# Optimization experiments

Measured on AMD Instinct MI355X. Metric: run time of the kernel, lower is better.

The kernel has to match this reference:

```python
import jax, jax.numpy as jnp
import numpy as np
from jax import lax

NEG = -1e9  # effective -inf, safe for fp32 and for gradients


def asg_loss(inputs, transitions, targets):
    """ASG criterion (wav2letter / gtn_applications semantics).

    inputs:      [B, T, N] emissions (log scores)
    transitions: [N+1, N]; transitions[0, i] = start score of class i,
                 transitions[i+1, j] = score of transition j -> i
    targets:     [B, L] int class ids (already replabel-packed + garbage-interleaved)
    Returns mean over batch of (logZ - forced_align_score) / L.
    """
    B, T, N = inputs.shape
    L = targets.shape[1]
    init = transitions[0]      # [N]
    trans = transitions[1:]    # [N, N], trans[i, j]: j -> i

    # ---- denominator: free recursion over all label sequences ----
    alpha0 = inputs[:, 0, :] + init  # [B, N]
    emis_t = jnp.swapaxes(inputs, 0, 1)  # [T, B, N]

    def den_step(alpha, e_t):
        # alpha[b, j] -> new alpha[b, i] = e_t[b, i] + LSE_j(alpha[b, j] + trans[i, j])
        a = jax.nn.logsumexp(alpha[:, None, :] + trans[None, :, :], axis=-1) + e_t
        return a, None

    alphaT, _ = lax.scan(den_step, alpha0, emis_t[1:])
    logZ = jax.nn.logsumexp(alphaT, axis=-1)  # [B]

    # ---- numerator: forced-alignment graph (self-loop or advance) ----
    # emissions gathered at target labels: [B, T, L]
    emis_y = jnp.take_along_axis(inputs, jnp.broadcast_to(targets[:, None, :], (B, T, L)), axis=2)
    stay_w = trans[targets, targets]                      # [B, L]   y_s -> y_s
    adv_w = trans[targets[:, 1:], targets[:, :-1]]        # [B, L-1] y_{s-1} -> y_s

    beta0 = jnp.full((B, L), NEG, dtype=inputs.dtype)
    beta0 = beta0.at[:, 0].set(init[targets[:, 0]] + emis_y[:, 0, 0])
    emis_y_t = jnp.swapaxes(emis_y, 0, 1)  # [T, B, L]

    def num_step(beta, e_t):
        stay = beta + stay_w
        adv = jnp.concatenate(
            [jnp.full((B, 1), NEG, dtype=beta.dtype), beta[:, :-1] + adv_w], axis=1)
        b = jnp.logaddexp(stay, adv) + e_t
        return b, None

    betaT, _ = lax.scan(num_step, beta0, emis_y_t[1:])
    target_score = betaT[:, -1]  # must end having consumed all L labels

    # reduction = 'mean': scale each sample by 1/len(target), then batch mean
    return jnp.mean((logZ - target_score) / L)


def setup_inputs() -> dict:
    key = jax.random.key(0)
    k1, k2, k3 = jax.random.split(key, 3)
    B, T, N, L = 128, 4000, 64, 101
    inputs = jax.random.normal(k1, (B, T, N), dtype=jnp.float32)
    transitions = jax.random.normal(k2, (N + 1, N), dtype=jnp.float32) * 0.1
    targets = jax.random.randint(k3, (B, L), 0, N, dtype=jnp.int64)
    return {"inputs": inputs, "transitions": transitions, "targets": targets}


def reference(inputs, transitions, targets):
    return asg_loss(inputs, transitions, targets)
```

## Files before the change

### kernel.cpp

```cpp
#include <hip/hip_runtime.h>


#define TT 4000
#define NN 64
#define LL 101
#define NSEG 64
#define SEGN 62
#define SLOTS 93

static constexpr float L2E  = 1.44269504088896340736f;
static constexpr float LN2F = 0.69314718055994530942f;
static constexpr float NEG2 = -1.0e30f;

#define WS_X    0
#define WS_NF   8192
#define WS_HB   22528
#define WS_LOSS 36864

#if defined(__has_builtin)
#if __has_builtin(__builtin_amdgcn_mfma_f32_16x16x16bf16_1k)
#define BF16MM 1
#endif
#if __has_builtin(__builtin_amdgcn_exp2f)
#define FEXP2(x) __builtin_amdgcn_exp2f(x)
#endif
#if __has_builtin(__builtin_amdgcn_logf)
#define FLOG2(x) __builtin_amdgcn_logf(x)
#endif
#endif
#ifndef FEXP2
#define FEXP2(x) exp2f(x)
#endif
#ifndef FLOG2
#define FLOG2(x) log2f(x)
#endif

typedef float f32x4 __attribute__((ext_vector_type(4)));
typedef short s16x4 __attribute__((ext_vector_type(4)));
typedef _Float16 h4 __attribute__((ext_vector_type(4)));

__device__ __forceinline__ unsigned cvt2(float a, float b) {
#ifdef BF16MM
  const unsigned ua = __builtin_bit_cast(unsigned, a);
  const unsigned ub = __builtin_bit_cast(unsigned, b);
  const unsigned ra = (ua + 0x7FFFu + ((ua >> 16) & 1u)) >> 16;
  const unsigned rb = (ub + 0x7FFFu + ((ub >> 16) & 1u)) >> 16;
  return ra | (rb << 16);
#else
  return __builtin_bit_cast(unsigned,
      __builtin_amdgcn_cvt_pkrtz(fminf(a, 3.0e4f), fminf(b, 3.0e4f)));
#endif
}

__device__ __forceinline__ f32x4 MM(uint2 a, uint2 b, f32x4 c) {
#ifdef BF16MM
  return __builtin_amdgcn_mfma_f32_16x16x16bf16_1k(
      __builtin_bit_cast(s16x4, a), __builtin_bit_cast(s16x4, b), c, 0, 0, 0);
#else
  return __builtin_amdgcn_mfma_f32_16x16x16f16(
      __builtin_bit_cast(h4, a), __builtin_bit_cast(h4, b), c, 0, 0, 0);
#endif
}

template<int CTRL>
__device__ __forceinline__ float dppf(float x) {
  return __builtin_bit_cast(float, __builtin_amdgcn_update_dpp(
      0, __builtin_bit_cast(int, x), CTRL, 0xf, 0xf, true));
}

__global__ __launch_bounds__(128) void asg_den(
    const float* __restrict__ E, const float* __restrict__ TR,
    float* __restrict__ ws)
{
  const int bid  = blockIdx.x;
  const int w    = threadIdx.x >> 6;
  const int lane = threadIdx.x & 63;
  const int b    = bid >> 1;
  const int p    = bid & 1;
  const int g4   = p * 2 + w;
  const float* em = E + (size_t)b * TT * NN;

  const int c = lane & 15, g = lane >> 4;
  const int j = g4 * 16 + c;

  uint2 Af[4][4];
#pragma unroll
  for (int rt = 0; rt < 4; ++rt)
#pragma unroll
    for (int kt = 0; kt < 4; ++kt) {
      const float* tr = TR + (size_t)(16 * rt + c + 1) * NN + 16 * kt + 4 * g;
      Af[rt][kt].x = cvt2(FEXP2(tr[0] * L2E), FEXP2(tr[1] * L2E));
      Af[rt][kt].y = cvt2(FEXP2(tr[2] * L2E), FEXP2(tr[3] * L2E));
    }

  f32x4 P[4];
#pragma unroll
  for (int rt = 0; rt < 4; ++rt)
#pragma unroll
    for (int e = 0; e < 4; ++e) {
      const int row = 16 * rt + 4 * g + e;
      P[rt][e] = (j == 0) ? FEXP2((em[row] + TR[row]) * L2E) : 1.0f;
    }

  float Csum = 0.f, snap = 0.f;
  const float* ebase = em + (size_t)(SEGN * j + 1) * NN + 4 * g;

#define COLSUM(dst) { float t_ =                                               \
    (P[0].x + P[0].y + P[0].z + P[0].w) + (P[1].x + P[1].y + P[1].z + P[1].w)  \
  + (P[2].x + P[2].y + P[2].z + P[2].w) + (P[3].x + P[3].y + P[3].z + P[3].w); \
  t_ += __shfl_xor(t_, 16); t_ += __shfl_xor(t_, 32);                          \
  (dst) = fmaxf(t_, 1e-30f); }

#define RENORM() { float cs_; COLSUM(cs_);                                     \
  const int mb_ = ((__builtin_bit_cast(int, cs_) >> 23) & 255) - 127;          \
  const float sc_ = __builtin_bit_cast(float, (127 - mb_) << 23);              \
  P[0] *= sc_; P[1] *= sc_; P[2] *= sc_; P[3] *= sc_;                          \
  Csum += (float)mb_; }

#define ELOAD(D, s_) { const int se_ = (s_) < (SLOTS - 1) ? (s_) : (SLOTS - 1);\
  const f32x4* p_ = (const f32x4*)(ebase + (size_t)se_ * NN);                  \
  D[0] = p_[0]; D[1] = p_[4]; D[2] = p_[8]; D[3] = p_[12]; }

#define STEP(M)                                                                \
  {                                                                            \
    uint2 Bf[4];                                                               \
    _Pragma("unroll") for (int kt = 0; kt < 4; ++kt) {                         \
      Bf[kt].x = cvt2(P[kt].x, P[kt].y);                                       \
      Bf[kt].y = cvt2(P[kt].z, P[kt].w);                                       \
    }                                                                          \
    _Pragma("unroll") for (int rt = 0; rt < 4; ++rt) {                         \
      f32x4 acc = {0.f, 0.f, 0.f, 0.f};                                        \
      acc = MM(Af[rt][0], Bf[0], acc);                                         \
      acc = MM(Af[rt][1], Bf[1], acc);                                         \
      acc = MM(Af[rt][2], Bf[2], acc);                                         \
      acc = MM(Af[rt][3], Bf[3], acc);                                         \
      _Pragma("unroll") for (int e = 0; e < 4; ++e)                            \
        P[rt][e] = fminf(fmaxf(                                                \
            acc[e] * FEXP2(fmaf(M[rt][e], L2E, -6.7f)), 1e-20f), 1e25f);       \
    }                                                                          \
  }

#define SUB(Ebuf, ss, kr)                                                      \
  { f32x4 T_[4] = {Ebuf[0], Ebuf[1], Ebuf[2], Ebuf[3]};                        \
    ELOAD(Ebuf, (ss) + 6);                                                     \
    STEP(T_);                                                                  \
    if ((ss) == 30) { float cs2_; COLSUM(cs2_);                                \
                      snap = Csum + FLOG2(cs2_) + 6.7f * 31.f; }               \
    if ((kr) == 5) RENORM(); }

  f32x4 E0[4], E1[4], E2[4], E3[4], E4[4], E5[4];
  ELOAD(E0, 0); ELOAD(E1, 1); ELOAD(E2, 2);
  ELOAD(E3, 3); ELOAD(E4, 4); ELOAD(E5, 5);

  for (int it = 0; it < 15; ++it) {
    const int s = 6 * it;
    SUB(E0, s, 0);     SUB(E1, s + 1, 1); SUB(E2, s + 2, 2);
    SUB(E3, s + 3, 3); SUB(E4, s + 4, 4); SUB(E5, s + 5, 5);
  }
  { f32x4 T_[4] = {E0[0], E0[1], E0[2], E0[3]}; STEP(T_); }
  { f32x4 T_[4] = {E1[0], E1[1], E1[2], E1[3]}; STEP(T_); }
  { f32x4 T_[4] = {E2[0], E2[1], E2[2], E2[3]}; STEP(T_); }

  float csf; COLSUM(csf);
  const float fin = Csum + FLOG2(csf) + 6.7f * (float)SLOTS;
  const float X = fin - ((j == 0) ? 0.f : snap);
  if (lane < 16) ws[WS_X + b * NSEG + g4 * 16 + lane] = X;

#undef SUB
#undef STEP
#undef ELOAD
#undef RENORM
#undef COLSUM
}

template<int DIR>
__device__ __forceinline__ void num_chain(const float* __restrict__ em,
                                          const float* __restrict__ TR,
                                          const int* __restrict__ Y,
                                          float* __restrict__ ws,
                                          const int b, const int l)
{
  const bool v0 = (2 * l     <= 100);
  const bool v1 = (2 * l + 1 <= 100);
  const int k0 = v0 ? 2 * l     : 100;
  const int k1 = v1 ? 2 * l + 1 : 100;
  const int y0 = Y[b * LL + k0];
  const int y1 = Y[b * LL + k1];
  const float SW0 = v0 ? FEXP2(TR[(y0 + 1) * NN + y0] * L2E) : 0.f;
  const float SW1 = v1 ? FEXP2(TR[(y1 + 1) * NN + y1] * L2E) : 0.f;
  float WLOC, WRECV, B0, B1, C;
  bool recvok;
  if (DIR == 0) {
    WLOC = v1 ? FEXP2(TR[(y1 + 1) * NN + y0] * L2E) : 0.f;
    const int ym0 = Y[b * LL + (k0 > 0 ? k0 - 1 : 0)];
    recvok = v0 && (l > 0);
    WRECV = recvok ? FEXP2(TR[(y0 + 1) * NN + ym0] * L2E) : 0.f;
    B0 = (l == 0) ? 1.f : 0.f;
    B1 = 0.f;
    C  = (l == 0) ? (TR[y0] + em[y0]) * L2E : 0.f;
  } else {
    WLOC = v1 ? FEXP2(TR[(y1 + 1) * NN + y0] * L2E) : 0.f;
    const int kp = (2 * l + 2 <= 100) ? 2 * l + 2 : 100;
    const int yp1 = Y[b * LL + kp];
    recvok = (2 * l + 2 <= 100);
    WRECV = recvok ? FEXP2(TR[(yp1 + 1) * NN + y1] * L2E) : 0.f;
    B0 = (l == 50) ? 1.f : 0.f;
    B1 = 0.f;
    C  = (l == 50) ? em[(size_t)(TT - 1) * NN + y0] * L2E : 0.f;
  }

#define TROW(t) ((size_t)((DIR == 0) ? (t) : (TT - 1 - (t))) * NN)
#define RADDR(t) em[TROW(((t) < 1999 ? (t) : 1999)) + l]

  float ring[48];
  float PE0[16], PE1[16];
  float ADJ = 0.f;

#define RESCALE()                                                              \
  {                                                                            \
    const float v_ = B0 + B1;                                                  \
    const int bits_ = __builtin_bit_cast(int, v_);                             \
    const int m_ = (v_ > 0.f) ? ((bits_ >> 23) & 255) - 127 : 0;               \
    const float sc_ = __builtin_bit_cast(float, (127 - m_) << 23);             \
    B0 *= sc_; B1 *= sc_; C += (float)m_;                                      \
    const float Cn_ = dppf<(DIR == 0) ? 0x138 : 0x130>(C);                     \
    const float dC_ = fminf(fmaxf(Cn_ - C, -120.f), 120.f);                    \
    ADJ = recvok ? FEXP2(dC_) * WRECV : 0.f;                                   \
  }

#define NSTEP2(E0v, E1v)                                                       \
  {                                                                            \
    if (DIR == 0) {                                                            \
      const float NB = dppf<0x138>(B1);                                        \
      const float t0 = fmaf(NB, ADJ, B0 * SW0);                                \
      const float t1 = fmaf(B0, WLOC, B1 * SW1);                               \
      B0 = t0 * (E0v); B1 = t1 * (E1v);                                        \
    } else {                                                                   \
      const float NB = dppf<0x130>(B0);                                        \
      const float t1 = fmaf(NB, ADJ, B1 * SW1);                                \
      const float t0 = fmaf(B1, WLOC, B0 * SW0);                               \
      B0 = t0 * (E0v); B1 = t1 * (E1v);                                        \
    }                                                                          \
  }

#pragma unroll
  for (int k = 0; k < 48; ++k) ring[(1 + k) % 48] = RADDR(1 + k);
#pragma unroll
  for (int t = 1; t <= 8; ++t) {
    const float r_ = ring[t % 48];
    PE0[t & 15] = FEXP2(__shfl(r_, y0) * L2E);
    PE1[t & 15] = FEXP2(__shfl(r_, y1) * L2E);
  }

#define QSTEP(k)                                                               \
  { if (((k) & 7) == 0) RESCALE();                                             \
    NSTEP2(PE0[(1 + (k)) & 15], PE1[(1 + (k)) & 15]);                          \
    { const float r_ = ring[(1 + (k) + 8) % 48];                               \
      PE0[(1 + (k) + 8) & 15] = FEXP2(__shfl(r_, y0) * L2E);                   \
      PE1[(1 + (k) + 8) & 15] = FEXP2(__shfl(r_, y1) * L2E); }                 \
    ring[(1 + (k)) % 48] = RADDR(tc + (k) + 48); }

#define Q4(k0)  QSTEP(k0) QSTEP((k0) + 1) QSTEP((k0) + 2) QSTEP((k0) + 3)
#define Q16(k0) Q4(k0) Q4((k0) + 4) Q4((k0) + 8) Q4((k0) + 12)

  for (int i = 0; i < 41; ++i) {
    const int tc = 1 + 48 * i;
    Q16(0) Q16(16) Q16(32)
  }
  {
    const int tc = 1969;
    Q16(0)
    Q4(16) Q4(20) Q4(24)
    QSTEP(28) QSTEP(29) QSTEP(30)
  }

#undef Q16
#undef Q4
#undef QSTEP
#undef NSTEP2
#undef RESCALE
#undef RADDR
#undef TROW

  const float o0 = (B0 > 1e-37f) ? C + FLOG2(B0) : NEG2;
  const float o1 = (B1 > 1e-37f) ? C + FLOG2(B1) : NEG2;
  const int base = (DIR ? WS_HB : WS_NF) + b * 112;
  if (v0) ws[base + 2 * l]     = o0;
  if (v1) ws[base + 2 * l + 1] = o1;
}

__global__ __launch_bounds__(64) void asg_num(
    const float* __restrict__ E, const float* __restrict__ TR,
    const int* __restrict__ Y, float* __restrict__ ws)
{
  const int bid = blockIdx.x;
  const int b   = bid >> 1;
  const int dir = bid & 1;
  const float* em = E + (size_t)b * TT * NN;
  if (dir == 0) num_chain<0>(em, TR, Y, ws, b, (int)threadIdx.x);
  else          num_chain<1>(em, TR, Y, ws, b, (int)threadIdx.x);
}

__global__ __launch_bounds__(128) void asg_combine(
    const float* __restrict__ TR, const int* __restrict__ Y,
    const float* __restrict__ ws, float* __restrict__ lossv)
{
  const int b = blockIdx.x;
  const int tid = threadIdx.x;
  __shared__ float sN[LL], sH[LL], red[128];
  __shared__ float sLogZ;

  if (tid == 0) {
    float z = 0.f;
    for (int s = 0; s < NSEG; ++s) z += ws[WS_X + b * NSEG + s];
    sLogZ = z;
  }
  if (tid < LL) { sN[tid] = ws[WS_NF + b * 112 + tid]; sH[tid] = ws[WS_HB + b * 112 + tid]; }
  __syncthreads();

  float val2 = -3.0e38f;
  if (tid < LL) {
    const int l = tid;
    const int y = Y[b * LL + l];
    const float s1 = sN[l] + TR[(y + 1) * NN + y] * L2E;
    float s2 = NEG2;
    if (l > 0) {
      const int ymm = Y[b * LL + l - 1];
      s2 = sN[l - 1] + TR[(y + 1) * NN + ymm] * L2E;
    }
    const float m = fmaxf(s1, s2);
    val2 = m + log2f(exp2f(s1 - m) + exp2f(s2 - m)) + sH[l];
  }
  red[tid] = val2;
  __syncthreads();
  if (tid == 0) {
    float m = red[0];
    for (int k = 1; k < LL; ++k) m = fmaxf(m, red[k]);
    float s = 0.f;
    for (int k = 0; k < LL; ++k) s += exp2f(red[k] - m);
    const float tgt2 = m + log2f(s);
    lossv[b] = (sLogZ - tgt2) * LN2F / (float)LL;
  }
}

__global__ __launch_bounds__(64) void asg_reduce(const float* __restrict__ lossv,
                                                 float* __restrict__ out)
{
  const int tid = threadIdx.x;
  float v = lossv[tid] + lossv[tid + 64];
  for (int off = 32; off; off >>= 1) v += __shfl_xor(v, off);
  if (tid == 0) out[0] = v * (1.0f / 128.0f);
}

extern "C" void kernel_launch(void* const* d_in, const int* in_sizes, int n_in,
                              void* d_out, int out_size, void* d_ws, size_t ws_size,
                              hipStream_t stream) {
  const float* E  = (const float*)d_in[0];
  const float* TR = (const float*)d_in[1];
  const int*   Y  = (const int*)d_in[2];
  float* out = (float*)d_out;
  float* ws  = (float*)d_ws;
  float* lossv = ws + WS_LOSS;

  asg_den<<<dim3(256), dim3(128), 0, stream>>>(E, TR, ws);
  asg_num<<<dim3(256), dim3(64), 0, stream>>>(E, TR, Y, ws);
  asg_combine<<<dim3(128), dim3(128), 0, stream>>>(TR, Y, ws, lossv);
  asg_reduce<<<dim3(1), dim3(64), 0, stream>>>(lossv, out);
}
```

Before: 153.0 us.

## Merge denominator and numerator kernels into one launch, direct-gather numerator loads

Combines the denominator MFMA kernel and the numerator chain kernel into a single 384-block launch. The numerator blocks now run both directions as two wavefronts in one block, so the two phases overlap across the GPU instead of running back to back. The numerator no longer loads full emission rows into a ring and shuffles out the target columns. Each lane now gathers its own two target emissions directly, using triple-buffered batches of 16 timesteps held in named registers. This removes the per-step shuffles and one kernel launch, at the cost of more scattered global loads and higher register pressure under launch_bounds(128,1).

```diff
diff --git a/kernel.cpp b/kernel.cpp
--- a/kernel.cpp
+++ b/kernel.cpp
@@ -66,111 +66,6 @@
 __device__ __forceinline__ float dppf(float x) {
   return __builtin_bit_cast(float, __builtin_amdgcn_update_dpp(
       0, __builtin_bit_cast(int, x), CTRL, 0xf, 0xf, true));
-}
-
-__global__ __launch_bounds__(128) void asg_den(
-    const float* __restrict__ E, const float* __restrict__ TR,
-    float* __restrict__ ws)
-{
-  const int bid  = blockIdx.x;
-  const int w    = threadIdx.x >> 6;
-  const int lane = threadIdx.x & 63;
-  const int b    = bid >> 1;
-  const int p    = bid & 1;
-  const int g4   = p * 2 + w;
-  const float* em = E + (size_t)b * TT * NN;
-
-  const int c = lane & 15, g = lane >> 4;
-  const int j = g4 * 16 + c;
-
-  uint2 Af[4][4];
-#pragma unroll
-  for (int rt = 0; rt < 4; ++rt)
-#pragma unroll
-    for (int kt = 0; kt < 4; ++kt) {
-      const float* tr = TR + (size_t)(16 * rt + c + 1) * NN + 16 * kt + 4 * g;
-      Af[rt][kt].x = cvt2(FEXP2(tr[0] * L2E), FEXP2(tr[1] * L2E));
-      Af[rt][kt].y = cvt2(FEXP2(tr[2] * L2E), FEXP2(tr[3] * L2E));
-    }
-
-  f32x4 P[4];
-#pragma unroll
-  for (int rt = 0; rt < 4; ++rt)
-#pragma unroll
-    for (int e = 0; e < 4; ++e) {
-      const int row = 16 * rt + 4 * g + e;
-      P[rt][e] = (j == 0) ? FEXP2((em[row] + TR[row]) * L2E) : 1.0f;
-    }
-
-  float Csum = 0.f, snap = 0.f;
-  const float* ebase = em + (size_t)(SEGN * j + 1) * NN + 4 * g;
-
-#define COLSUM(dst) { float t_ =                                               \
-    (P[0].x + P[0].y + P[0].z + P[0].w) + (P[1].x + P[1].y + P[1].z + P[1].w)  \
-  + (P[2].x + P[2].y + P[2].z + P[2].w) + (P[3].x + P[3].y + P[3].z + P[3].w); \
-  t_ += __shfl_xor(t_, 16); t_ += __shfl_xor(t_, 32);                          \
-  (dst) = fmaxf(t_, 1e-30f); }
-
-#define RENORM() { float cs_; COLSUM(cs_);                                     \
-  const int mb_ = ((__builtin_bit_cast(int, cs_) >> 23) & 255) - 127;          \
-  const float sc_ = __builtin_bit_cast(float, (127 - mb_) << 23);              \
-  P[0] *= sc_; P[1] *= sc_; P[2] *= sc_; P[3] *= sc_;                          \
-  Csum += (float)mb_; }
-
-#define ELOAD(D, s_) { const int se_ = (s_) < (SLOTS - 1) ? (s_) : (SLOTS - 1);\
-  const f32x4* p_ = (const f32x4*)(ebase + (size_t)se_ * NN);                  \
-  D[0] = p_[0]; D[1] = p_[4]; D[2] = p_[8]; D[3] = p_[12]; }
-
-#define STEP(M)                                                                \
-  {                                                                            \
-    uint2 Bf[4];                                                               \
-    _Pragma("unroll") for (int kt = 0; kt < 4; ++kt) {                         \
-      Bf[kt].x = cvt2(P[kt].x, P[kt].y);                                       \
-      Bf[kt].y = cvt2(P[kt].z, P[kt].w);                                       \
-    }                                                                          \
-    _Pragma("unroll") for (int rt = 0; rt < 4; ++rt) {                         \
-      f32x4 acc = {0.f, 0.f, 0.f, 0.f};                                        \
-      acc = MM(Af[rt][0], Bf[0], acc);                                         \
-      acc = MM(Af[rt][1], Bf[1], acc);                                         \
-      acc = MM(Af[rt][2], Bf[2], acc);                                         \
-      acc = MM(Af[rt][3], Bf[3], acc);                                         \
-      _Pragma("unroll") for (int e = 0; e < 4; ++e)                            \
-        P[rt][e] = fminf(fmaxf(                                                \
-            acc[e] * FEXP2(fmaf(M[rt][e], L2E, -6.7f)), 1e-20f), 1e25f);       \
-    }                                                                          \
-  }
-
-#define SUB(Ebuf, ss, kr)                                                      \
-  { f32x4 T_[4] = {Ebuf[0], Ebuf[1], Ebuf[2], Ebuf[3]};                        \
-    ELOAD(Ebuf, (ss) + 6);                                                     \
-    STEP(T_);                                                                  \
-    if ((ss) == 30) { float cs2_; COLSUM(cs2_);                                \
-                      snap = Csum + FLOG2(cs2_) + 6.7f * 31.f; }               \
-    if ((kr) == 5) RENORM(); }
-
-  f32x4 E0[4], E1[4], E2[4], E3[4], E4[4], E5[4];
-  ELOAD(E0, 0); ELOAD(E1, 1); ELOAD(E2, 2);
-  ELOAD(E3, 3); ELOAD(E4, 4); ELOAD(E5, 5);
-
-  for (int it = 0; it < 15; ++it) {
-    const int s = 6 * it;
-    SUB(E0, s, 0);     SUB(E1, s + 1, 1); SUB(E2, s + 2, 2);
-    SUB(E3, s + 3, 3); SUB(E4, s + 4, 4); SUB(E5, s + 5, 5);
-  }
-  { f32x4 T_[4] = {E0[0], E0[1], E0[2], E0[3]}; STEP(T_); }
-  { f32x4 T_[4] = {E1[0], E1[1], E1[2], E1[3]}; STEP(T_); }
-  { f32x4 T_[4] = {E2[0], E2[1], E2[2], E2[3]}; STEP(T_); }
-
-  float csf; COLSUM(csf);
-  const float fin = Csum + FLOG2(csf) + 6.7f * (float)SLOTS;
-  const float X = fin - ((j == 0) ? 0.f : snap);
-  if (lane < 16) ws[WS_X + b * NSEG + g4 * 16 + lane] = X;
-
-#undef SUB
-#undef STEP
-#undef ELOAD
-#undef RENORM
-#undef COLSUM
 }
 
 template<int DIR>
@@ -209,11 +104,9 @@
     C  = (l == 50) ? em[(size_t)(TT - 1) * NN + y0] * L2E : 0.f;
   }
 
-#define TROW(t) ((size_t)((DIR == 0) ? (t) : (TT - 1 - (t))) * NN)
-#define RADDR(t) em[TROW(((t) < 1999 ? (t) : 1999)) + l]
-
-  float ring[48];
-  float PE0[16], PE1[16];
+  constexpr int ST = (DIR == 0) ? NN : -NN;
+#define TROW0(t) ((long)((DIR == 0) ? (t) : (TT - 1 - (t))) * NN)
+
   float ADJ = 0.f;
 
 #define RESCALE()                                                              \
@@ -243,44 +136,64 @@
     }                                                                          \
   }
 
-#pragma unroll
-  for (int k = 0; k < 48; ++k) ring[(1 + k) % 48] = RADDR(1 + k);
-#pragma unroll
-  for (int t = 1; t <= 8; ++t) {
-    const float r_ = ring[t % 48];
-    PE0[t & 15] = FEXP2(__shfl(r_, y0) * L2E);
-    PE1[t & 15] = FEXP2(__shfl(r_, y1) * L2E);
-  }
-
-#define QSTEP(k)                                                               \
-  { if (((k) & 7) == 0) RESCALE();                                             \
-    NSTEP2(PE0[(1 + (k)) & 15], PE1[(1 + (k)) & 15]);                          \
-    { const float r_ = ring[(1 + (k) + 8) % 48];                               \
-      PE0[(1 + (k) + 8) & 15] = FEXP2(__shfl(r_, y0) * L2E);                   \
-      PE1[(1 + (k) + 8) & 15] = FEXP2(__shfl(r_, y1) * L2E); }                 \
-    ring[(1 + (k)) % 48] = RADDR(tc + (k) + 48); }
-
-#define Q4(k0)  QSTEP(k0) QSTEP((k0) + 1) QSTEP((k0) + 2) QSTEP((k0) + 3)
-#define Q16(k0) Q4(k0) Q4((k0) + 4) Q4((k0) + 8) Q4((k0) + 12)
+#define NB_DECL(Bk)                                                            \
+  float Bk##0a, Bk##0b, Bk##1a, Bk##1b, Bk##2a, Bk##2b, Bk##3a, Bk##3b,        \
+        Bk##4a, Bk##4b, Bk##5a, Bk##5b, Bk##6a, Bk##6b, Bk##7a, Bk##7b,        \
+        Bk##8a, Bk##8b, Bk##9a, Bk##9b, Bk##10a, Bk##10b, Bk##11a, Bk##11b,    \
+        Bk##12a, Bk##12b, Bk##13a, Bk##13b, Bk##14a, Bk##14b, Bk##15a, Bk##15b;
+
+  NB_DECL(KA) NB_DECL(KB) NB_DECL(KC)
+
+#define NLD(Bk, k)                                                             \
+  Bk##k##a = p0_[(k) * ST];                                                    \
+  Bk##k##b = p1_[(k) * ST];
+
+#define NISSUE(Bk, ts)                                                         \
+  { const float* p0_ = em + TROW0(ts) + y0;                                    \
+    const float* p1_ = em + TROW0(ts) + y1;                                    \
+    NLD(Bk,0)  NLD(Bk,1)  NLD(Bk,2)  NLD(Bk,3)                                 \
+    NLD(Bk,4)  NLD(Bk,5)  NLD(Bk,6)  NLD(Bk,7)                                 \
+    NLD(Bk,8)  NLD(Bk,9)  NLD(Bk,10) NLD(Bk,11)                                \
+    NLD(Bk,12) NLD(Bk,13) NLD(Bk,14) NLD(Bk,15) }
+
+#define NRUN1(Bk, k)                                                           \
+  { const float E0_ = FEXP2(Bk##k##a * L2E);                                   \
+    const float E1_ = FEXP2(Bk##k##b * L2E);                                   \
+    NSTEP2(E0_, E1_); }
+
+#define NRUN8A(Bk) RESCALE();                                                  \
+  NRUN1(Bk,0) NRUN1(Bk,1) NRUN1(Bk,2) NRUN1(Bk,3)                              \
+  NRUN1(Bk,4) NRUN1(Bk,5) NRUN1(Bk,6) NRUN1(Bk,7)
+#define NRUN8B(Bk) RESCALE();                                                  \
+  NRUN1(Bk,8)  NRUN1(Bk,9)  NRUN1(Bk,10) NRUN1(Bk,11)                          \
+  NRUN1(Bk,12) NRUN1(Bk,13) NRUN1(Bk,14) NRUN1(Bk,15)
+#define NRUN16(Bk) NRUN8A(Bk) NRUN8B(Bk)
+
+  NISSUE(KA, 1)
+  NISSUE(KB, 17)
 
   for (int i = 0; i < 41; ++i) {
     const int tc = 1 + 48 * i;
-    Q16(0) Q16(16) Q16(32)
-  }
-  {
-    const int tc = 1969;
-    Q16(0)
-    Q4(16) Q4(20) Q4(24)
-    QSTEP(28) QSTEP(29) QSTEP(30)
-  }
-
-#undef Q16
-#undef Q4
-#undef QSTEP
+    NISSUE(KC, tc + 32)  NRUN16(KA)
+    NISSUE(KA, tc + 48)  NRUN16(KB)
+    NISSUE(KB, tc + 64)  NRUN16(KC)
+  }
+  NRUN16(KA)
+  NRUN8A(KB)
+  RESCALE();
+  NRUN1(KB,8) NRUN1(KB,9) NRUN1(KB,10) NRUN1(KB,11)
+  NRUN1(KB,12) NRUN1(KB,13) NRUN1(KB,14)
+
+#undef NRUN16
+#undef NRUN8B
+#undef NRUN8A
+#undef NRUN1
+#undef NISSUE
+#undef NLD
+#undef NB_DECL
 #undef NSTEP2
 #undef RESCALE
-#undef RADDR
-#undef TROW
+#undef TROW0
 
   const float o0 = (B0 > 1e-37f) ? C + FLOG2(B0) : NEG2;
   const float o1 = (B1 > 1e-37f) ? C + FLOG2(B1) : NEG2;
@@ -289,16 +202,118 @@
   if (v1) ws[base + 2 * l + 1] = o1;
 }
 
-__global__ __launch_bounds__(64) void asg_num(
+__global__ __launch_bounds__(128, 1) void asg_main(
     const float* __restrict__ E, const float* __restrict__ TR,
     const int* __restrict__ Y, float* __restrict__ ws)
 {
-  const int bid = blockIdx.x;
-  const int b   = bid >> 1;
-  const int dir = bid & 1;
-  const float* em = E + (size_t)b * TT * NN;
-  if (dir == 0) num_chain<0>(em, TR, Y, ws, b, (int)threadIdx.x);
-  else          num_chain<1>(em, TR, Y, ws, b, (int)threadIdx.x);
+  const int bid  = blockIdx.x;
+  const int w    = threadIdx.x >> 6;
+  const int lane = threadIdx.x & 63;
+
+  if (bid < 256) {
+    const int b    = bid >> 1;
+    const int p    = bid & 1;
+    const int g4   = p * 2 + w;
+    const float* em = E + (size_t)b * TT * NN;
+
+    const int c = lane & 15, g = lane >> 4;
+    const int j = g4 * 16 + c;
+
+    uint2 Af[4][4];
+#pragma unroll
+    for (int rt = 0; rt < 4; ++rt)
+#pragma unroll
+      for (int kt = 0; kt < 4; ++kt) {
+        const float* tr = TR + (size_t)(16 * rt + c + 1) * NN + 16 * kt + 4 * g;
+        Af[rt][kt].x = cvt2(FEXP2(tr[0] * L2E), FEXP2(tr[1] * L2E));
+        Af[rt][kt].y = cvt2(FEXP2(tr[2] * L2E), FEXP2(tr[3] * L2E));
+      }
+
+    f32x4 P[4];
+#pragma unroll
+    for (int rt = 0; rt < 4; ++rt)
+#pragma unroll
+      for (int e = 0; e < 4; ++e) {
+        const int row = 16 * rt + 4 * g + e;
+        P[rt][e] = (j == 0) ? FEXP2((em[row] + TR[row]) * L2E) : 1.0f;
+      }
+
+    float Csum = 0.f, snap = 0.f;
+    const float* ebase = em + (size_t)(SEGN * j + 1) * NN + 4 * g;
+
+#define COLSUM(dst) { float t_ =                                               \
+    (P[0].x + P[0].y + P[0].z + P[0].w) + (P[1].x + P[1].y + P[1].z + P[1].w)  \
+  + (P[2].x + P[2].y + P[2].z + P[2].w) + (P[3].x + P[3].y + P[3].z + P[3].w); \
+  t_ += __shfl_xor(t_, 16); t_ += __shfl_xor(t_, 32);                          \
+  (dst) = fmaxf(t_, 1e-30f); }
+
+#define RENORM() { float cs_; COLSUM(cs_);                                     \
+  const int mb_ = ((__builtin_bit_cast(int, cs_) >> 23) & 255) - 127;          \
+  const float sc_ = __builtin_bit_cast(float, (127 - mb_) << 23);              \
+  P[0] *= sc_; P[1] *= sc_; P[2] *= sc_; P[3] *= sc_;                          \
+  Csum += (float)mb_; }
+
+#define ELOAD(D, s_) { const int se_ = (s_) < (SLOTS - 1) ? (s_) : (SLOTS - 1);\
+  const f32x4* p_ = (const f32x4*)(ebase + (size_t)se_ * NN);                  \
+  D[0] = p_[0]; D[1] = p_[4]; D[2] = p_[8]; D[3] = p_[12]; }
+
+#define STEP(M)                                                                \
+  {                                                                            \
+    uint2 Bf[4];                                                               \
+    _Pragma("unroll") for (int kt = 0; kt < 4; ++kt) {                         \
+      Bf[kt].x = cvt2(P[kt].x, P[kt].y);                                       \
+      Bf[kt].y = cvt2(P[kt].z, P[kt].w);                                       \
+    }                                                                          \
+    _Pragma("unroll") for (int rt = 0; rt < 4; ++rt) {                         \
+      f32x4 acc = {0.f, 0.f, 0.f, 0.f};                                        \
+      acc = MM(Af[rt][0], Bf[0], acc);                                         \
+      acc = MM(Af[rt][1], Bf[1], acc);                                         \
+      acc = MM(Af[rt][2], Bf[2], acc);                                         \
+      acc = MM(Af[rt][3], Bf[3], acc);                                         \
+      _Pragma("unroll") for (int e = 0; e < 4; ++e)                            \
+        P[rt][e] = fminf(fmaxf(                                                \
+            acc[e] * FEXP2(fmaf(M[rt][e], L2E, -6.7f)), 1e-20f), 1e25f);       \
+    }                                                                          \
+  }
+
+#define SUB(Ebuf, ss, kr)                                                      \
+  { f32x4 T_[4] = {Ebuf[0], Ebuf[1], Ebuf[2], Ebuf[3]};                        \
+    ELOAD(Ebuf, (ss) + 6);                                                     \
+    STEP(T_);                                                                  \
+    if ((ss) == 30) { float cs2_; COLSUM(cs2_);                                \
+                      snap = Csum + FLOG2(cs2_) + 6.7f * 31.f; }               \
+    if ((kr) == 5) RENORM(); }
+
+    f32x4 E0[4], E1[4], E2[4], E3[4], E4[4], E5[4];
+    ELOAD(E0, 0); ELOAD(E1, 1); ELOAD(E2, 2);
+    ELOAD(E3, 3); ELOAD(E4, 4); ELOAD(E5, 5);
+
+    for (int it = 0; it < 15; ++it) {
+      const int s = 6 * it;
+      SUB(E0, s, 0);     SUB(E1, s + 1, 1); SUB(E2, s + 2, 2);
+      SUB(E3, s + 3, 3); SUB(E4, s + 4, 4); SUB(E5, s + 5, 5);
+    }
+    { f32x4 T_[4] = {E0[0], E0[1], E0[2], E0[3]}; STEP(T_); }
+    { f32x4 T_[4] = {E1[0], E1[1], E1[2], E1[3]}; STEP(T_); }
+    { f32x4 T_[4] = {E2[0], E2[1], E2[2], E2[3]}; STEP(T_); }
+
+    float csf; COLSUM(csf);
+    const float fin = Csum + FLOG2(csf) + 6.7f * (float)SLOTS;
+    const float X = fin - ((j == 0) ? 0.f : snap);
+    if (lane < 16) ws[WS_X + b * NSEG + g4 * 16 + lane] = X;
+
+#undef SUB
+#undef STEP
+#undef ELOAD
+#undef RENORM
+#undef COLSUM
+
+  } else {
+    const int b = bid - 256;
+    const float* em = E + (size_t)b * TT * NN;
+    if (w == 0) num_chain<0>(em, TR, Y, ws, b, lane);
+    else        num_chain<1>(em, TR, Y, ws, b, lane);
+  }
 }
 
 __global__ __launch_bounds__(128) void asg_combine(
@@ -362,8 +377,7 @@
   float* ws  = (float*)d_ws;
   float* lossv = ws + WS_LOSS;
 
-  asg_den<<<dim3(256), dim3(128), 0, stream>>>(E, TR, ws);
-  asg_num<<<dim3(256), dim3(64), 0, stream>>>(E, TR, Y, ws);
+  asg_main<<<dim3(384), dim3(128), 0, stream>>>(E, TR, Y, ws);
   asg_combine<<<dim3(128), dim3(128), 0, stream>>>(TR, Y, ws, lossv);
   asg_reduce<<<dim3(1), dim3(64), 0, stream>>>(lossv, out);
 }
```

Measured after the change: 127.9 us. 16.4% less time.

## Fuse denominator and numerator kernels and interleave forward/backward numerator chains

Applied to the files above, without the earlier changes.

Merges the denominator and numerator kernels into one launch of 384 blocks, so the numerator blocks run alongside the denominator blocks instead of after them. Each numerator wave now runs both the forward and backward chains interleaved, which gives two independent dependency chains to hide latency. It gathers emissions directly at the label columns with double-buffered 16-step register loads, replacing the ring buffer plus shuffles. It also swaps round-to-nearest bf16 conversion for truncation and drops the upper clamp in the denominator step, trading some precision and overflow safety for fewer instructions.

```diff
diff --git a/kernel.cpp b/kernel.cpp
--- a/kernel.cpp
+++ b/kernel.cpp
@@ -52,6 +52,17 @@
 #endif
 }
 
+__device__ __forceinline__ unsigned cvt2t(float a, float b) {
+#ifdef BF16MM
+  const unsigned ua = __builtin_bit_cast(unsigned, a);
+  const unsigned ub = __builtin_bit_cast(unsigned, b);
+  return (ua >> 16) | (ub & 0xFFFF0000u);
+#else
+  return __builtin_bit_cast(unsigned,
+      __builtin_amdgcn_cvt_pkrtz(fminf(a, 3.0e4f), fminf(b, 3.0e4f)));
+#endif
+}
+
 __device__ __forceinline__ f32x4 MM(uint2 a, uint2 b, f32x4 c) {
 #ifdef BF16MM
   return __builtin_amdgcn_mfma_f32_16x16x16bf16_1k(
@@ -68,42 +79,44 @@
       0, __builtin_bit_cast(int, x), CTRL, 0xf, 0xf, true));
 }
 
-__global__ __launch_bounds__(128) void asg_den(
+__global__ __launch_bounds__(128, 1) void asg_main(
     const float* __restrict__ E, const float* __restrict__ TR,
-    float* __restrict__ ws)
+    const int* __restrict__ Y, float* __restrict__ ws)
 {
   const int bid  = blockIdx.x;
   const int w    = threadIdx.x >> 6;
   const int lane = threadIdx.x & 63;
-  const int b    = bid >> 1;
-  const int p    = bid & 1;
-  const int g4   = p * 2 + w;
-  const float* em = E + (size_t)b * TT * NN;
-
-  const int c = lane & 15, g = lane >> 4;
-  const int j = g4 * 16 + c;
-
-  uint2 Af[4][4];
+
+  if (bid < 256) {
+    const int b    = bid >> 1;
+    const int p    = bid & 1;
+    const int g4   = p * 2 + w;
+    const float* em = E + (size_t)b * TT * NN;
+
+    const int c = lane & 15, g = lane >> 4;
+    const int j = g4 * 16 + c;
+
+    uint2 Af[4][4];
 #pragma unroll
-  for (int rt = 0; rt < 4; ++rt)
+    for (int rt = 0; rt < 4; ++rt)
 #pragma unroll
-    for (int kt = 0; kt < 4; ++kt) {
-      const float* tr = TR + (size_t)(16 * rt + c + 1) * NN + 16 * kt + 4 * g;
-      Af[rt][kt].x = cvt2(FEXP2(tr[0] * L2E), FEXP2(tr[1] * L2E));
-      Af[rt][kt].y = cvt2(FEXP2(tr[2] * L2E), FEXP2(tr[3] * L2E));
-    }
-
-  f32x4 P[4];
+      for (int kt = 0; kt < 4; ++kt) {
+        const float* tr = TR + (size_t)(16 * rt + c + 1) * NN + 16 * kt + 4 * g;
+        Af[rt][kt].x = cvt2(FEXP2(tr[0] * L2E), FEXP2(tr[1] * L2E));
+        Af[rt][kt].y = cvt2(FEXP2(tr[2] * L2E), FEXP2(tr[3] * L2E));
+      }
+
+    f32x4 P[4];
 #pragma unroll
-  for (int rt = 0; rt < 4; ++rt)
+    for (int rt = 0; rt < 4; ++rt)
 #pragma unroll
-    for (int e = 0; e < 4; ++e) {
-      const int row = 16 * rt + 4 * g + e;
-      P[rt][e] = (j == 0) ? FEXP2((em[row] + TR[row]) * L2E) : 1.0f;
-    }
-
-  float Csum = 0.f, snap = 0.f;
-  const float* ebase = em + (size_t)(SEGN * j + 1) * NN + 4 * g;
+      for (int e = 0; e < 4; ++e) {
+        const int row = 16 * rt + 4 * g + e;
+        P[rt][e] = (j == 0) ? FEXP2((em[row] + TR[row]) * L2E) : 1.0f;
+      }
+
+    float Csum = 0.f, snap = 0.f;
+    const float* ebase = em + (size_t)(SEGN * j + 1) * NN + 4 * g;
 
 #define COLSUM(dst) { float t_ =                                               \
     (P[0].x + P[0].y + P[0].z + P[0].w) + (P[1].x + P[1].y + P[1].z + P[1].w)  \
@@ -125,8 +138,8 @@
   {                                                                            \
     uint2 Bf[4];                                                               \
     _Pragma("unroll") for (int kt = 0; kt < 4; ++kt) {                         \
-      Bf[kt].x = cvt2(P[kt].x, P[kt].y);                                       \
-      Bf[kt].y = cvt2(P[kt].z, P[kt].w);                                       \
+      Bf[kt].x = cvt2t(P[kt].x, P[kt].y);                                      \
+      Bf[kt].y = cvt2t(P[kt].z, P[kt].w);                                      \
     }                                                                          \
     _Pragma("unroll") for (int rt = 0; rt < 4; ++rt) {                         \
       f32x4 acc = {0.f, 0.f, 0.f, 0.f};                                        \
@@ -135,8 +148,7 @@
       acc = MM(Af[rt][2], Bf[2], acc);                                         \
       acc = MM(Af[rt][3], Bf[3], acc);                                         \
       _Pragma("unroll") for (int e = 0; e < 4; ++e)                            \
-        P[rt][e] = fminf(fmaxf(                                                \
-            acc[e] * FEXP2(fmaf(M[rt][e], L2E, -6.7f)), 1e-20f), 1e25f);       \
+        P[rt][e] = fmaxf(acc[e] * FEXP2(fmaf(M[rt][e], L2E, -6.7f)), 1e-20f);  \
     }                                                                          \
   }
 
@@ -148,157 +160,155 @@
                       snap = Csum + FLOG2(cs2_) + 6.7f * 31.f; }               \
     if ((kr) == 5) RENORM(); }
 
-  f32x4 E0[4], E1[4], E2[4], E3[4], E4[4], E5[4];
-  ELOAD(E0, 0); ELOAD(E1, 1); ELOAD(E2, 2);
-  ELOAD(E3, 3); ELOAD(E4, 4); ELOAD(E5, 5);
-
-  for (int it = 0; it < 15; ++it) {
-    const int s = 6 * it;
-    SUB(E0, s, 0);     SUB(E1, s + 1, 1); SUB(E2, s + 2, 2);
-    SUB(E3, s + 3, 3); SUB(E4, s + 4, 4); SUB(E5, s + 5, 5);
-  }
-  { f32x4 T_[4] = {E0[0], E0[1], E0[2], E0[3]}; STEP(T_); }
-  { f32x4 T_[4] = {E1[0], E1[1], E1[2], E1[3]}; STEP(T_); }
-  { f32x4 T_[4] = {E2[0], E2[1], E2[2], E2[3]}; STEP(T_); }
-
-  float csf; COLSUM(csf);
-  const float fin = Csum + FLOG2(csf) + 6.7f * (float)SLOTS;
-  const float X = fin - ((j == 0) ? 0.f : snap);
-  if (lane < 16) ws[WS_X + b * NSEG + g4 * 16 + lane] = X;
+    f32x4 E0[4], E1[4], E2[4], E3[4], E4[4], E5[4];
+    ELOAD(E0, 0); ELOAD(E1, 1); ELOAD(E2, 2);
+    ELOAD(E3, 3); ELOAD(E4, 4); ELOAD(E5, 5);
+
+    for (int it = 0; it < 15; ++it) {
+      const int s = 6 * it;
+      SUB(E0, s, 0);     SUB(E1, s + 1, 1); SUB(E2, s + 2, 2);
+      SUB(E3, s + 3, 3); SUB(E4, s + 4, 4); SUB(E5, s + 5, 5);
+    }
+    { f32x4 T_[4] = {E0[0], E0[1], E0[2], E0[3]}; STEP(T_); }
+    { f32x4 T_[4] = {E1[0], E1[1], E1[2], E1[3]}; STEP(T_); }
+    { f32x4 T_[4] = {E2[0], E2[1], E2[2], E2[3]}; STEP(T_); }
+
+    float csf; COLSUM(csf);
+    const float fin = Csum + FLOG2(csf) + 6.7f * (float)SLOTS;
+    const float X = fin - ((j == 0) ? 0.f : snap);
+    if (lane < 16) ws[WS_X + b * NSEG + g4 * 16 + lane] = X;
 
 #undef SUB
 #undef STEP
 #undef ELOAD
 #undef RENORM
 #undef COLSUM
-}
-
-template<int DIR>
-__device__ __forceinline__ void num_chain(const float* __restrict__ em,
-                                          const float* __restrict__ TR,
-                                          const int* __restrict__ Y,
-                                          float* __restrict__ ws,
-                                          const int b, const int l)
-{
-  const bool v0 = (2 * l     <= 100);
-  const bool v1 = (2 * l + 1 <= 100);
-  const int k0 = v0 ? 2 * l     : 100;
-  const int k1 = v1 ? 2 * l + 1 : 100;
-  const int y0 = Y[b * LL + k0];
-  const int y1 = Y[b * LL + k1];
-  const float SW0 = v0 ? FEXP2(TR[(y0 + 1) * NN + y0] * L2E) : 0.f;
-  const float SW1 = v1 ? FEXP2(TR[(y1 + 1) * NN + y1] * L2E) : 0.f;
-  float WLOC, WRECV, B0, B1, C;
-  bool recvok;
-  if (DIR == 0) {
-    WLOC = v1 ? FEXP2(TR[(y1 + 1) * NN + y0] * L2E) : 0.f;
+
+  } else {
+    if (w != 0) return;
+    const int b = bid - 256;
+    const int l = lane;
+    const float* em = E + (size_t)b * TT * NN;
+
+    const bool v0 = (2 * l     <= 100);
+    const bool v1 = (2 * l + 1 <= 100);
+    const int k0 = v0 ? 2 * l     : 100;
+    const int k1 = v1 ? 2 * l + 1 : 100;
+    const int y0 = Y[b * LL + k0];
+    const int y1 = Y[b * LL + k1];
+    const float SW0 = v0 ? FEXP2(TR[(y0 + 1) * NN + y0] * L2E) : 0.f;
+    const float SW1 = v1 ? FEXP2(TR[(y1 + 1) * NN + y1] * L2E) : 0.f;
+    const float WLOC = v1 ? FEXP2(TR[(y1 + 1) * NN + y0] * L2E) : 0.f;
+
     const int ym0 = Y[b * LL + (k0 > 0 ? k0 - 1 : 0)];
-    recvok = v0 && (l > 0);
-    WRECV = recvok ? FEXP2(TR[(y0 + 1) * NN + ym0] * L2E) : 0.f;
-    B0 = (l == 0) ? 1.f : 0.f;
-    B1 = 0.f;
-    C  = (l == 0) ? (TR[y0] + em[y0]) * L2E : 0.f;
-  } else {
-    WLOC = v1 ? FEXP2(TR[(y1 + 1) * NN + y0] * L2E) : 0.f;
+    const bool frecv = v0 && (l > 0);
+    const float FWRECV = frecv ? FEXP2(TR[(y0 + 1) * NN + ym0] * L2E) : 0.f;
+    float FB0 = (l == 0) ? 1.f : 0.f;
+    float FB1 = 0.f;
+    float FC  = (l == 0) ? (TR[y0] + em[y0]) * L2E : 0.f;
+    float FADJ = 0.f;
+
     const int kp = (2 * l + 2 <= 100) ? 2 * l + 2 : 100;
     const int yp1 = Y[b * LL + kp];
-    recvok = (2 * l + 2 <= 100);
-    WRECV = recvok ? FEXP2(TR[(yp1 + 1) * NN + y1] * L2E) : 0.f;
-    B0 = (l == 50) ? 1.f : 0.f;
-    B1 = 0.f;
-    C  = (l == 50) ? em[(size_t)(TT - 1) * NN + y0] * L2E : 0.f;
-  }
-
-#define TROW(t) ((size_t)((DIR == 0) ? (t) : (TT - 1 - (t))) * NN)
-#define RADDR(t) em[TROW(((t) < 1999 ? (t) : 1999)) + l]
-
-  float ring[48];
-  float PE0[16], PE1[16];
-  float ADJ = 0.f;
-
-#define RESCALE()                                                              \
-  {                                                                            \
-    const float v_ = B0 + B1;                                                  \
+    const bool grecv = (2 * l + 2 <= 100);
+    const float GWRECV = grecv ? FEXP2(TR[(yp1 + 1) * NN + y1] * L2E) : 0.f;
+    float GB0 = (l == 50) ? 1.f : 0.f;
+    float GB1 = 0.f;
+    float GC  = (l == 50) ? em[(size_t)(TT - 1) * NN + y0] * L2E : 0.f;
+    float GADJ = 0.f;
+
+#define FOR16(M, P) M(P,0) M(P,1) M(P,2) M(P,3) M(P,4) M(P,5) M(P,6) M(P,7)    \
+                    M(P,8) M(P,9) M(P,10) M(P,11) M(P,12) M(P,13) M(P,14) M(P,15)
+#define DECL1(P, k) float P##k##a, P##k##b;
+    FOR16(DECL1, FA) FOR16(DECL1, FB) FOR16(DECL1, GA) FOR16(DECL1, GB)
+
+#define LDF1(P, k) P##k##a = q0_[(k) * NN]; P##k##b = q1_[(k) * NN];
+#define ISSF(P, ts) { const float* q0_ = em + (size_t)(ts) * NN + y0;          \
+                      const float* q1_ = em + (size_t)(ts) * NN + y1;          \
+                      FOR16(LDF1, P) }
+#define LDG1(P, k) P##k##a = q0_[-(k) * NN]; P##k##b = q1_[-(k) * NN];
+#define ISSG(P, ts) { const float* q0_ = em + (size_t)(TT - 1 - (ts)) * NN + y0;\
+                      const float* q1_ = em + (size_t)(TT - 1 - (ts)) * NN + y1;\
+                      FOR16(LDG1, P) }
+
+#define FRESC()                                                                \
+  { const float v_ = FB0 + FB1;                                                \
     const int bits_ = __builtin_bit_cast(int, v_);                             \
     const int m_ = (v_ > 0.f) ? ((bits_ >> 23) & 255) - 127 : 0;               \
     const float sc_ = __builtin_bit_cast(float, (127 - m_) << 23);             \
-    B0 *= sc_; B1 *= sc_; C += (float)m_;                                      \
-    const float Cn_ = dppf<(DIR == 0) ? 0x138 : 0x130>(C);                     \
-    const float dC_ = fminf(fmaxf(Cn_ - C, -120.f), 120.f);                    \
-    ADJ = recvok ? FEXP2(dC_) * WRECV : 0.f;                                   \
-  }
-
-#define NSTEP2(E0v, E1v)                                                       \
-  {                                                                            \
-    if (DIR == 0) {                                                            \
-      const float NB = dppf<0x138>(B1);                                        \
-      const float t0 = fmaf(NB, ADJ, B0 * SW0);                                \
-      const float t1 = fmaf(B0, WLOC, B1 * SW1);                               \
-      B0 = t0 * (E0v); B1 = t1 * (E1v);                                        \
-    } else {                                                                   \
-      const float NB = dppf<0x130>(B0);                                        \
-      const float t1 = fmaf(NB, ADJ, B1 * SW1);                                \
-      const float t0 = fmaf(B1, WLOC, B0 * SW0);                               \
-      B0 = t0 * (E0v); B1 = t1 * (E1v);                                        \
-    }                                                                          \
-  }
-
-#pragma unroll
-  for (int k = 0; k < 48; ++k) ring[(1 + k) % 48] = RADDR(1 + k);
-#pragma unroll
-  for (int t = 1; t <= 8; ++t) {
-    const float r_ = ring[t % 48];
-    PE0[t & 15] = FEXP2(__shfl(r_, y0) * L2E);
-    PE1[t & 15] = FEXP2(__shfl(r_, y1) * L2E);
-  }
-
-#define QSTEP(k)                                                               \
-  { if (((k) & 7) == 0) RESCALE();                                             \
-    NSTEP2(PE0[(1 + (k)) & 15], PE1[(1 + (k)) & 15]);                          \
-    { const float r_ = ring[(1 + (k) + 8) % 48];                               \
-      PE0[(1 + (k) + 8) & 15] = FEXP2(__shfl(r_, y0) * L2E);                   \
-      PE1[(1 + (k) + 8) & 15] = FEXP2(__shfl(r_, y1) * L2E); }                 \
-    ring[(1 + (k)) % 48] = RADDR(tc + (k) + 48); }
-
-#define Q4(k0)  QSTEP(k0) QSTEP((k0) + 1) QSTEP((k0) + 2) QSTEP((k0) + 3)
-#define Q16(k0) Q4(k0) Q4((k0) + 4) Q4((k0) + 8) Q4((k0) + 12)
-
-  for (int i = 0; i < 41; ++i) {
-    const int tc = 1 + 48 * i;
-    Q16(0) Q16(16) Q16(32)
-  }
-  {
-    const int tc = 1969;
-    Q16(0)
-    Q4(16) Q4(20) Q4(24)
-    QSTEP(28) QSTEP(29) QSTEP(30)
-  }
-
-#undef Q16
-#undef Q4
-#undef QSTEP
-#undef NSTEP2
-#undef RESCALE
-#undef RADDR
-#undef TROW
-
-  const float o0 = (B0 > 1e-37f) ? C + FLOG2(B0) : NEG2;
-  const float o1 = (B1 > 1e-37f) ? C + FLOG2(B1) : NEG2;
-  const int base = (DIR ? WS_HB : WS_NF) + b * 112;
-  if (v0) ws[base + 2 * l]     = o0;
-  if (v1) ws[base + 2 * l + 1] = o1;
-}
-
-__global__ __launch_bounds__(64) void asg_num(
-    const float* __restrict__ E, const float* __restrict__ TR,
-    const int* __restrict__ Y, float* __restrict__ ws)
-{
-  const int bid = blockIdx.x;
-  const int b   = bid >> 1;
-  const int dir = bid & 1;
-  const float* em = E + (size_t)b * TT * NN;
-  if (dir == 0) num_chain<0>(em, TR, Y, ws, b, (int)threadIdx.x);
-  else          num_chain<1>(em, TR, Y, ws, b, (int)threadIdx.x);
+    FB0 *= sc_; FB1 *= sc_; FC += (float)m_;                                   \
+    const float Cn_ = dppf<0x138>(FC);                                         \
+    const float dC_ = fminf(fmaxf(Cn_ - FC, -120.f), 120.f);                   \
+    FADJ = frecv ? FEXP2(dC_) * FWRECV : 0.f; }
+
+#define GRESC()                                                                \
+  { const float v_ = GB0 + GB1;                                                \
+    const int bits_ = __builtin_bit_cast(int, v_);                             \
+    const int m_ = (v_ > 0.f) ? ((bits_ >> 23) & 255) - 127 : 0;               \
+    const float sc_ = __builtin_bit_cast(float, (127 - m_) << 23);             \
+    GB0 *= sc_; GB1 *= sc_; GC += (float)m_;                                   \
+    const float Cn_ = dppf<0x130>(GC);                                         \
+    const float dC_ = fminf(fmaxf(Cn_ - GC, -120.f), 120.f);                   \
+    GADJ = grecv ? FEXP2(dC_) * GWRECV : 0.f; }
+
+#define PRUN1(PF, PG, k)                                                       \
+  { const float fe0 = FEXP2(PF##k##a * L2E);                                   \
+    const float fe1 = FEXP2(PF##k##b * L2E);                                   \
+    const float ge0 = FEXP2(PG##k##a * L2E);                                   \
+    const float ge1 = FEXP2(PG##k##b * L2E);                                   \
+    { const float NB = dppf<0x138>(FB1);                                       \
+      const float t0 = fmaf(NB, FADJ, FB0 * SW0);                              \
+      const float t1 = fmaf(FB0, WLOC, FB1 * SW1);                             \
+      FB0 = t0 * fe0; FB1 = t1 * fe1; }                                        \
+    { const float NB = dppf<0x130>(GB0);                                       \
+      const float t1 = fmaf(NB, GADJ, GB1 * SW1);                              \
+      const float t0 = fmaf(GB1, WLOC, GB0 * SW0);                             \
+      GB0 = t0 * ge0; GB1 = t1 * ge1; } }
+
+#define PRUN8A(PF, PG) FRESC() GRESC()                                         \
+  PRUN1(PF,PG,0) PRUN1(PF,PG,1) PRUN1(PF,PG,2) PRUN1(PF,PG,3)                  \
+  PRUN1(PF,PG,4) PRUN1(PF,PG,5) PRUN1(PF,PG,6) PRUN1(PF,PG,7)
+#define PRUN8B(PF, PG) FRESC() GRESC()                                         \
+  PRUN1(PF,PG,8)  PRUN1(PF,PG,9)  PRUN1(PF,PG,10) PRUN1(PF,PG,11)              \
+  PRUN1(PF,PG,12) PRUN1(PF,PG,13) PRUN1(PF,PG,14) PRUN1(PF,PG,15)
+#define PRUN16(PF, PG) PRUN8A(PF, PG) PRUN8B(PF, PG)
+
+    ISSF(FA, 1) ISSG(GA, 1)
+
+    for (int i = 0; i < 62; ++i) {
+      const int tc = 1 + 32 * i;
+      ISSF(FB, tc + 16) ISSG(GB, tc + 16)
+      PRUN16(FA, GA)
+      ISSF(FA, tc + 32) ISSG(GA, tc + 32)
+      PRUN16(FB, GB)
+    }
+    PRUN8A(FA, GA)
+    FRESC() GRESC()
+    PRUN1(FA,GA,8)  PRUN1(FA,GA,9)  PRUN1(FA,GA,10) PRUN1(FA,GA,11)
+    PRUN1(FA,GA,12) PRUN1(FA,GA,13) PRUN1(FA,GA,14)
+
+#undef PRUN16
+#undef PRUN8B
+#undef PRUN8A
+#undef PRUN1
+#undef GRESC
+#undef FRESC
+#undef ISSG
+#undef LDG1
+#undef ISSF
+#undef LDF1
+#undef DECL1
+#undef FOR16
+
+    const float fo0 = (FB0 > 1e-37f) ? FC + FLOG2(FB0) : NEG2;
+    const float fo1 = (FB1 > 1e-37f) ? FC + FLOG2(FB1) : NEG2;
+    const float go0 = (GB0 > 1e-37f) ? GC + FLOG2(GB0) : NEG2;
+    const float go1 = (GB1 > 1e-37f) ? GC + FLOG2(GB1) : NEG2;
+    if (v0) { ws[WS_NF + b * 112 + 2 * l]     = fo0;
+              ws[WS_HB + b * 112 + 2 * l]     = go0; }
+    if (v1) { ws[WS_NF + b * 112 + 2 * l + 1] = fo1;
+              ws[WS_HB + b * 112 + 2 * l + 1] = go1; }
+  }
 }
 
 __global__ __launch_bounds__(128) void asg_combine(
@@ -362,8 +372,7 @@
   float* ws  = (float*)d_ws;
   float* lossv = ws + WS_LOSS;
 
-  asg_den<<<dim3(256), dim3(128), 0, stream>>>(E, TR, ws);
-  asg_num<<<dim3(256), dim3(64), 0, stream>>>(E, TR, Y, ws);
+  asg_main<<<dim3(384), dim3(128), 0, stream>>>(E, TR, Y, ws);
   asg_combine<<<dim3(128), dim3(128), 0, stream>>>(TR, Y, ws, lossv);
   asg_reduce<<<dim3(1), dim3(64), 0, stream>>>(lossv, out);
 }
```

Result: slower. 181.2 us (+18.5%).
